# Kernel tuning notes

Measured on AMD Instinct MI355X. Metric: run time of the kernel, lower is better.

## Reference

```python
import jax, jax.numpy as jnp
import numpy as np

FEATURE_DIM = 512
DEPTH = 128
NUM_CLASSES = 1000


def setup_inputs() -> dict:
    key = jax.random.key(0)
    ks = jax.random.split(key, 9)
    s = 1.0 / np.sqrt(FEATURE_DIM)
    sd = 1.0 / np.sqrt(DEPTH)
    return {
        "x": jax.random.normal(ks[0], (8, 2048, FEATURE_DIM), dtype=jnp.float32),
        "Wq": jax.random.uniform(ks[1], (FEATURE_DIM, DEPTH), jnp.float32, -s, s),
        "bq": jax.random.uniform(ks[2], (DEPTH,), jnp.float32, -s, s),
        "Wk": jax.random.uniform(ks[3], (FEATURE_DIM, DEPTH), jnp.float32, -s, s),
        "bk": jax.random.uniform(ks[4], (DEPTH,), jnp.float32, -s, s),
        "Wv": jax.random.uniform(ks[5], (FEATURE_DIM, DEPTH), jnp.float32, -s, s),
        "bv": jax.random.uniform(ks[6], (DEPTH,), jnp.float32, -s, s),
        "Wl": jax.random.uniform(ks[7], (DEPTH, NUM_CLASSES), jnp.float32, -sd, sd),
        "bl": jax.random.uniform(ks[8], (NUM_CLASSES,), jnp.float32, -sd, sd),
    }


def reference(x, Wq, bq, Wk, bk, Wv, bv, Wl, bl):
    # q,k,v: [B,S,depth]
    q = jnp.einsum("bsf,fd->bsd", x, Wq) + bq
    k = jnp.einsum("bsf,fd->bsd", x, Wk) + bk
    v = jnp.einsum("bsf,fd->bsd", x, Wv) + bv
    # NOTE: original applies no 1/sqrt(depth) scaling
    logit = jnp.einsum("bqd,bkd->bqk", q, k)  # [B,S,S]
    attn = jax.nn.softmax(logit, axis=2)
    attn_out = jnp.einsum("bqk,bkd->bqd", attn, v)  # [B,S,depth]
    out = jnp.einsum("bsd,dc->bsc", attn_out, Wl) + bl  # [B,S,C]
    return out.mean(axis=1)  # [B,C]
```

## Files before the change

kernel.cpp:

```cpp
#include <hip/hip_runtime.h>
#include <stdint.h>

#define NB 8
#define SS 2048
#define FF 512
#define DD 128
#define CC 1000
#define KC 8
#define CHUNK (SS / KC)

typedef __attribute__((ext_vector_type(8))) short bf16x8;
typedef __attribute__((ext_vector_type(4))) float f32x4;

__device__ __forceinline__ short f2bf(float f) {
    uint32_t u;
    __builtin_memcpy(&u, &f, 4);
    u = (u + 0x7fffu + ((u >> 16) & 1u)) >> 16;
    return (short)u;
}
__device__ __forceinline__ float bf2f(short h) {
    uint32_t u = ((uint32_t)(uint16_t)h) << 16;
    float f;
    __builtin_memcpy(&f, &u, 4);
    return f;
}
__device__ __forceinline__ void async16(const void* g, void* l) {
    __builtin_amdgcn_global_load_lds(
        (const __attribute__((address_space(1))) uint32_t*)g,
        (__attribute__((address_space(3))) uint32_t*)l, 16, 0, 0);
}

__global__ void prep(const float* __restrict__ x,
                     const float* __restrict__ Wq, const float* __restrict__ Wk,
                     const float* __restrict__ Wv,
                     short* __restrict__ xb, short* __restrict__ Wt)
{
    int bx = blockIdx.x;
    if (bx < 4096) {
        int id = bx * 256 + threadIdx.x;
        const float4* src = (const float4*)x + id * 2;
        float4 a = src[0], b2 = src[1];
        bf16x8 o;
        o[0] = f2bf(a.x);  o[1] = f2bf(a.y);  o[2] = f2bf(a.z);  o[3] = f2bf(a.w);
        o[4] = f2bf(b2.x); o[5] = f2bf(b2.y); o[6] = f2bf(b2.z); o[7] = f2bf(b2.w);
        *(bf16x8*)(xb + id * 8) = o;
    } else {
        int id = (bx - 4096) * 256 + threadIdx.x;
        int w = id >> 16, rem = id & 65535;
        int n = rem >> 9, kx = rem & 511;
        const float* Wsrc = (w == 0) ? Wq : (w == 1) ? Wk : Wv;
        Wt[w * 65536 + n * 512 + kx] = f2bf(Wsrc[kx * 128 + n]);
    }
}

__global__ __launch_bounds__(256) void qkv_proj(
    const short* __restrict__ xb, const short* __restrict__ Wt,
    const float* __restrict__ bq, const float* __restrict__ bk, const float* __restrict__ bv,
    short* __restrict__ qo, short* __restrict__ ko, short* __restrict__ vto)
{
    __shared__ __align__(16) short As[128 * 64];
    __shared__ __align__(16) short Bs[128 * 64];

    const int m0   = blockIdx.x * 128;
    const int mat  = blockIdx.y;
    const int tid  = threadIdx.x;
    const int wave = tid >> 6, lane = tid & 63;
    const int quad = lane >> 4, l16 = lane & 15;
    const int wr = wave >> 1, wc = wave & 1;

    const short* Wm = Wt + mat * 65536;

    f32x4 acc[4][4];
    for (int i = 0; i < 4; i++)
        for (int j = 0; j < 4; j++) acc[i][j] = (f32x4){0.f, 0.f, 0.f, 0.f};

    const int sr = lane >> 3;
    const int sc = (lane & 7) ^ (sr & 7);

    for (int kk = 0; kk < 512; kk += 64) {
        __syncthreads();
        for (int i = 0; i < 4; i++) {
            int ins = wave * 4 + i;
            int r = ins * 8 + sr;
            async16(xb + (m0 + r) * 512 + kk + sc * 8, &As[ins * 512]);
            async16(Wm + r * 512 + kk + sc * 8,        &Bs[ins * 512]);
        }
        __syncthreads();

        for (int kc = 0; kc < 2; kc++) {
            bf16x8 af[4], bfr[4];
            for (int mt = 0; mt < 4; mt++) {
                int R = wr * 64 + mt * 16 + l16, cc = kc * 4 + quad;
                af[mt] = *(const bf16x8*)&As[(R * 8 + (cc ^ (R & 7))) * 8];
            }
            for (int nt = 0; nt < 4; nt++) {
                int R = wc * 64 + nt * 16 + l16, cc = kc * 4 + quad;
                bfr[nt] = *(const bf16x8*)&Bs[(R * 8 + (cc ^ (R & 7))) * 8];
            }
            for (int mt = 0; mt < 4; mt++)
                for (int nt = 0; nt < 4; nt++)
                    acc[mt][nt] = __builtin_amdgcn_mfma_f32_16x16x32_bf16(
                        af[mt], bfr[nt], acc[mt][nt], 0, 0, 0);
        }
    }

    const float* bias = (mat == 0) ? bq : (mat == 1) ? bk : bv;
    for (int mt = 0; mt < 4; mt++) {
        int grow_base = m0 + wr * 64 + mt * 16 + quad * 4;
        for (int nt = 0; nt < 4; nt++) {
            int col = wc * 64 + nt * 16 + l16;
            float bb = bias[col];
            for (int r = 0; r < 4; r++) {
                int grow = grow_base + r;
                short h = f2bf(acc[mt][nt][r] + bb);
                if (mat == 0)      qo[grow * 128 + col] = h;
                else if (mat == 1) ko[grow * 128 + col] = h;
                else {
                    int b_ = grow >> 11, si = grow & 2047;
                    vto[(b_ * 128 + col) * 2048 + si] = h;
                }
            }
        }
    }
}

__global__ __launch_bounds__(256) void attn_l(
    const short* __restrict__ q, const short* __restrict__ k,
    float* __restrict__ l_part)
{
    __shared__ __align__(16) short ks[64 * 128];

    const int b  = blockIdx.y;
    const int q0 = blockIdx.x * 128;
    const int lq = blockIdx.z;
    const int c0 = lq * CHUNK;
    const int tid  = threadIdx.x;
    const int wave = tid >> 6, lane = tid & 63;
    const int quad = lane >> 4, l16 = lane & 15;

    bf16x8 qf[2][4];
    for (int m = 0; m < 2; m++)
        for (int c = 0; c < 4; c++)
            qf[m][c] = *(const bf16x8*)(q + (b * 2048 + q0 + wave * 32 + m * 16 + l16) * 128
                                          + c * 32 + quad * 8);

    float lsum[2][4] = {{0.f,0.f,0.f,0.f},{0.f,0.f,0.f,0.f}};
    const int krl = lane >> 4;

    for (int s0 = c0; s0 < c0 + CHUNK; s0 += 64) {
        __syncthreads();
        for (int i = 0; i < 4; i++) {
            int ik = wave * 4 + i;
            int kr = ik * 4 + krl;
            int kc8 = (lane & 15) ^ (kr & 15);
            async16(k + (b * 2048 + s0 + kr) * 128 + kc8 * 8, &ks[ik * 512]);
        }
        __syncthreads();

        for (int ct = 0; ct < 4; ct++) {
            f32x4 Sf[2];
            Sf[0] = (f32x4){0.f,0.f,0.f,0.f};
            Sf[1] = (f32x4){0.f,0.f,0.f,0.f};
            int R = ct * 16 + l16;
            for (int c = 0; c < 4; c++) {
                int cc = c * 4 + quad;
                bf16x8 kb = *(const bf16x8*)&ks[(R * 16 + (cc ^ l16)) * 8];
                for (int m = 0; m < 2; m++)
                    Sf[m] = __builtin_amdgcn_mfma_f32_16x16x32_bf16(
                        qf[m][c], kb, Sf[m], 0, 0, 0);
            }
            for (int m = 0; m < 2; m++)
                for (int r = 0; r < 4; r++)
                    lsum[m][r] += __expf(Sf[m][r] - 10.0f);
        }
    }

    for (int m = 0; m < 2; m++)
        for (int r = 0; r < 4; r++) {
            float lv = lsum[m][r];
            lv += __shfl_xor(lv, 1);
            lv += __shfl_xor(lv, 2);
            lv += __shfl_xor(lv, 4);
            lv += __shfl_xor(lv, 8);
            if (l16 == 0)
                l_part[(lq * 8 + b) * 2048 + q0 + wave * 32 + m * 16 + quad * 4 + r] = lv;
        }
}

__global__ __launch_bounds__(256) void attn_w(
    const short* __restrict__ q, const short* __restrict__ k,
    const float* __restrict__ l_part, float* __restrict__ w)
{
    __shared__ __align__(16) short ks[64 * 128];
    __shared__ float wl[4][256];

    const int b  = blockIdx.y;
    const int q0 = blockIdx.x * 128;
    const int lq = blockIdx.z;
    const int c0 = lq * CHUNK;
    const int tid  = threadIdx.x;
    const int wave = tid >> 6, lane = tid & 63;
    const int quad = lane >> 4, l16 = lane & 15;

    bf16x8 qf[2][4];
    for (int m = 0; m < 2; m++)
        for (int c = 0; c < 4; c++)
            qf[m][c] = *(const bf16x8*)(q + (b * 2048 + q0 + wave * 32 + m * 16 + l16) * 128
                                          + c * 32 + quad * 8);

    float linv[2][4];
    for (int m = 0; m < 2; m++)
        for (int r = 0; r < 4; r++) {
            int row = q0 + wave * 32 + m * 16 + quad * 4 + r;
            float lt = 0.f;
            for (int kc = 0; kc < KC; kc++) lt += l_part[(kc * 8 + b) * 2048 + row];
            linv[m][r] = 1.0f / lt;
        }

    const int krl = lane >> 4;

    for (int s0 = c0; s0 < c0 + CHUNK; s0 += 64) {
        __syncthreads();
        for (int i = 0; i < 4; i++) {
            int ik = wave * 4 + i;
            int kr = ik * 4 + krl;
            int kc8 = (lane & 15) ^ (kr & 15);
            async16(k + (b * 2048 + s0 + kr) * 128 + kc8 * 8, &ks[ik * 512]);
        }
        __syncthreads();

        for (int ct = 0; ct < 4; ct++) {
            f32x4 Sf[2];
            Sf[0] = (f32x4){0.f,0.f,0.f,0.f};
            Sf[1] = (f32x4){0.f,0.f,0.f,0.f};
            int R = ct * 16 + l16;
            for (int c = 0; c < 4; c++) {
                int cc = c * 4 + quad;
                bf16x8 kb = *(const bf16x8*)&ks[(R * 16 + (cc ^ l16)) * 8];
                for (int m = 0; m < 2; m++)
                    Sf[m] = __builtin_amdgcn_mfma_f32_16x16x32_bf16(
                        qf[m][c], kb, Sf[m], 0, 0, 0);
            }
            float cs = 0.f;
            for (int m = 0; m < 2; m++)
                for (int r = 0; r < 4; r++)
                    cs += __expf(Sf[m][r] - 10.0f) * linv[m][r];
            cs += __shfl_xor(cs, 16);
            cs += __shfl_xor(cs, 32);
            if (quad == 0) wl[wave][(s0 - c0) + ct * 16 + l16] = cs;
        }
    }

    __syncthreads();
    {
        float s = wl[0][tid] + wl[1][tid] + wl[2][tid] + wl[3][tid];
        atomicAdd(&w[b * 2048 + c0 + tid], s);
    }
}

__global__ void wv(const float* __restrict__ w, const short* __restrict__ vt,
                   float* __restrict__ accum)
{
    const int b  = blockIdx.x;
    const int dg = blockIdx.y;
    const int tid = threadIdx.x;
    const int d  = dg * 16 + (tid >> 4);
    const int sr = (tid & 15) * 128;
    const float* wb = w + b * 2048 + sr;
    const short* vp = vt + (size_t)(b * 128 + d) * 2048 + sr;
    float s = 0.f;
    for (int i = 0; i < 128; i += 8) {
        bf16x8 v8 = *(const bf16x8*)(vp + i);
        for (int j = 0; j < 8; j++) s += wb[i + j] * bf2f(v8[j]);
    }
    s += __shfl_xor(s, 1);
    s += __shfl_xor(s, 2);
    s += __shfl_xor(s, 4);
    s += __shfl_xor(s, 8);
    if ((tid & 15) == 0) accum[b * 128 + d] = s;
}

__global__ void final_proj(const float* __restrict__ accum, const float* __restrict__ Wl,
                           const float* __restrict__ bl, float* __restrict__ out)
{
    int id = blockIdx.x * 256 + threadIdx.x;
    if (id >= NB * CC) return;
    int b = id / CC, c = id % CC;
    float s = 0.f;
    for (int d = 0; d < 128; d++)
        s += accum[b * 128 + d] * Wl[d * 1000 + c];
    out[id] = s * (1.0f / 2048.0f) + bl[c];
}

extern "C" void kernel_launch(void* const* d_in, const int* in_sizes, int n_in,
                              void* d_out, int out_size, void* d_ws, size_t ws_size,
                              hipStream_t stream) {
    const float* x  = (const float*)d_in[0];
    const float* Wq = (const float*)d_in[1];
    const float* bq = (const float*)d_in[2];
    const float* Wk = (const float*)d_in[3];
    const float* bk = (const float*)d_in[4];
    const float* Wv = (const float*)d_in[5];
    const float* bv = (const float*)d_in[6];
    const float* Wl = (const float*)d_in[7];
    const float* bl = (const float*)d_in[8];
    float* out = (float*)d_out;

    char* ws = (char*)d_ws;
    short* qo     = (short*)(ws);
    short* ko     = (short*)(ws + 4194304);
    short* vto    = (short*)(ws + 8388608);
    short* xb     = (short*)(ws + 12582912);
    short* Wt     = (short*)(ws + 29360128);
    float* l_part = (float*)(ws + 29753344);
    float* wbuf   = (float*)(ws + 30277632);
    float* acc    = (float*)(ws + 30343168);

    hipMemsetAsync(wbuf, 0, (size_t)NB * SS * sizeof(float), stream);
    prep<<<4864, 256, 0, stream>>>(x, Wq, Wk, Wv, xb, Wt);
    qkv_proj<<<dim3(128, 3), 256, 0, stream>>>(xb, Wt, bq, bk, bv, qo, ko, vto);
    attn_l<<<dim3(16, 8, KC), 256, 0, stream>>>(qo, ko, l_part);
    attn_w<<<dim3(16, 8, KC), 256, 0, stream>>>(qo, ko, l_part, wbuf);
    wv<<<dim3(8, 8), 256, 0, stream>>>(wbuf, vto, acc);
    final_proj<<<(NB * CC + 255) / 256, 256, 0, stream>>>(acc, Wl, bl, out);
}
```

Baseline: 160.8 us.

## Replace w atomics and memset with partial buffers; store V row-major

attn_w now writes per-query-tile partial column weights to a buffer instead of issuing atomicAdds, and wv sums those 16 partials. This removes the memset launch and the global atomics. V is now stored row-major rather than transposed, which avoids the strided scattered stores in qkv_proj. wv is restructured to read row-major V with coalesced accesses and to atomically accumulate into accum, which attn_l zeroes. The cost is extra partial-buffer traffic and atomics in wv.

```diff
diff --git a/kernel.cpp b/kernel.cpp
--- a/kernel.cpp
+++ b/kernel.cpp
@@ -56,7 +56,7 @@
 __global__ __launch_bounds__(256) void qkv_proj(
     const short* __restrict__ xb, const short* __restrict__ Wt,
     const float* __restrict__ bq, const float* __restrict__ bk, const float* __restrict__ bv,
-    short* __restrict__ qo, short* __restrict__ ko, short* __restrict__ vto)
+    short* __restrict__ qo, short* __restrict__ ko, short* __restrict__ vo)
 {
     __shared__ __align__(16) short As[128 * 64];
     __shared__ __align__(16) short Bs[128 * 64];
@@ -105,28 +105,21 @@
     }
 
     const float* bias = (mat == 0) ? bq : (mat == 1) ? bk : bv;
+    short* outp = (mat == 0) ? qo : (mat == 1) ? ko : vo;
     for (int mt = 0; mt < 4; mt++) {
         int grow_base = m0 + wr * 64 + mt * 16 + quad * 4;
         for (int nt = 0; nt < 4; nt++) {
             int col = wc * 64 + nt * 16 + l16;
             float bb = bias[col];
-            for (int r = 0; r < 4; r++) {
-                int grow = grow_base + r;
-                short h = f2bf(acc[mt][nt][r] + bb);
-                if (mat == 0)      qo[grow * 128 + col] = h;
-                else if (mat == 1) ko[grow * 128 + col] = h;
-                else {
-                    int b_ = grow >> 11, si = grow & 2047;
-                    vto[(b_ * 128 + col) * 2048 + si] = h;
-                }
-            }
+            for (int r = 0; r < 4; r++)
+                outp[(grow_base + r) * 128 + col] = f2bf(acc[mt][nt][r] + bb);
         }
     }
 }
 
 __global__ __launch_bounds__(256) void attn_l(
     const short* __restrict__ q, const short* __restrict__ k,
-    float* __restrict__ l_part)
+    float* __restrict__ l_part, float* __restrict__ accum)
 {
     __shared__ __align__(16) short ks[64 * 128];
 
@@ -137,6 +130,11 @@
     const int tid  = threadIdx.x;
     const int wave = tid >> 6, lane = tid & 63;
     const int quad = lane >> 4, l16 = lane & 15;
+
+    if (blockIdx.x == 0 && blockIdx.y == 0 && blockIdx.z == 0) {
+        accum[tid] = 0.f; accum[256 + tid] = 0.f;
+        accum[512 + tid] = 0.f; accum[768 + tid] = 0.f;
+    }
 
     bf16x8 qf[2][4];
     for (int m = 0; m < 2; m++)
@@ -189,13 +187,14 @@
 
 __global__ __launch_bounds__(256) void attn_w(
     const short* __restrict__ q, const short* __restrict__ k,
-    const float* __restrict__ l_part, float* __restrict__ w)
+    const float* __restrict__ l_part, float* __restrict__ w_part)
 {
     __shared__ __align__(16) short ks[64 * 128];
     __shared__ float wl[4][256];
 
     const int b  = blockIdx.y;
-    const int q0 = blockIdx.x * 128;
+    const int qt = blockIdx.x;
+    const int q0 = qt * 128;
     const int lq = blockIdx.z;
     const int c0 = lq * CHUNK;
     const int tid  = threadIdx.x;
@@ -254,30 +253,31 @@
     __syncthreads();
     {
         float s = wl[0][tid] + wl[1][tid] + wl[2][tid] + wl[3][tid];
-        atomicAdd(&w[b * 2048 + c0 + tid], s);
-    }
-}
-
-__global__ void wv(const float* __restrict__ w, const short* __restrict__ vt,
+        w_part[(qt * 8 + b) * 2048 + c0 + tid] = s;
+    }
+}
+
+__global__ void wv(const float* __restrict__ w_part, const short* __restrict__ vo,
                    float* __restrict__ accum)
 {
-    const int b  = blockIdx.x;
-    const int dg = blockIdx.y;
-    const int tid = threadIdx.x;
-    const int d  = dg * 16 + (tid >> 4);
-    const int sr = (tid & 15) * 128;
-    const float* wb = w + b * 2048 + sr;
-    const short* vp = vt + (size_t)(b * 128 + d) * 2048 + sr;
-    float s = 0.f;
-    for (int i = 0; i < 128; i += 8) {
-        bf16x8 v8 = *(const bf16x8*)(vp + i);
-        for (int j = 0; j < 8; j++) s += wb[i + j] * bf2f(v8[j]);
-    }
-    s += __shfl_xor(s, 1);
-    s += __shfl_xor(s, 2);
-    s += __shfl_xor(s, 4);
-    s += __shfl_xor(s, 8);
-    if ((tid & 15) == 0) accum[b * 128 + d] = s;
+    __shared__ float wsh[256];
+    const int b    = blockIdx.x;
+    const int slab = blockIdx.y;
+    const int tid  = threadIdx.x;
+
+    int s = slab * 256 + tid;
+    float wsum = 0.f;
+    for (int qt = 0; qt < 16; qt++) wsum += w_part[(qt * 8 + b) * 2048 + s];
+    wsh[tid] = wsum;
+    __syncthreads();
+
+    const int d = tid & 127, h = tid >> 7;
+    float a = 0.f;
+    for (int i = 0; i < 128; i++) {
+        int sl = h * 128 + i;
+        a += wsh[sl] * bf2f(vo[(size_t)(b * 2048 + slab * 256 + sl) * 128 + d]);
+    }
+    atomicAdd(&accum[b * 128 + d], a);
 }
 
 __global__ void final_proj(const float* __restrict__ accum, const float* __restrict__ Wl,
@@ -309,18 +309,17 @@
     char* ws = (char*)d_ws;
     short* qo     = (short*)(ws);
     short* ko     = (short*)(ws + 4194304);
-    short* vto    = (short*)(ws + 8388608);
+    short* vo     = (short*)(ws + 8388608);
     short* xb     = (short*)(ws + 12582912);
     short* Wt     = (short*)(ws + 29360128);
     float* l_part = (float*)(ws + 29753344);
-    float* wbuf   = (float*)(ws + 30277632);
-    float* acc    = (float*)(ws + 30343168);
-
-    hipMemsetAsync(wbuf, 0, (size_t)NB * SS * sizeof(float), stream);
+    float* w_part = (float*)(ws + 30277632);
+    float* acc    = (float*)(ws + 31326208);
+
     prep<<<4864, 256, 0, stream>>>(x, Wq, Wk, Wv, xb, Wt);
-    qkv_proj<<<dim3(128, 3), 256, 0, stream>>>(xb, Wt, bq, bk, bv, qo, ko, vto);
-    attn_l<<<dim3(16, 8, KC), 256, 0, stream>>>(qo, ko, l_part);
-    attn_w<<<dim3(16, 8, KC), 256, 0, stream>>>(qo, ko, l_part, wbuf);
-    wv<<<dim3(8, 8), 256, 0, stream>>>(wbuf, vto, acc);
+    qkv_proj<<<dim3(128, 3), 256, 0, stream>>>(xb, Wt, bq, bk, bv, qo, ko, vo);
+    attn_l<<<dim3(16, 8, KC), 256, 0, stream>>>(qo, ko, l_part, acc);
+    attn_w<<<dim3(16, 8, KC), 256, 0, stream>>>(qo, ko, l_part, w_part);
+    wv<<<dim3(8, 8), 256, 0, stream>>>(w_part, vo, acc);
     final_proj<<<(NB * CC + 255) / 256, 256, 0, stream>>>(acc, Wl, bl, out);
 }
```

Result: faster. 153.2 us (median of 2 runs) (-4.7%).
